# Performance work log

Hardware: AMD Instinct MI355X
Metric: run time of the kernel (lower is better)

Reference implementation:

```python
import jax, jax.numpy as jnp
import numpy as np


def setup_inputs() -> dict:
    key = jax.random.key(0)
    k1, k2 = jax.random.split(key)
    B, C, H, W = 8, 19, 512, 1024
    preds = jax.random.normal(k1, (B, C, H, W), dtype=jnp.float32)
    targets = jax.random.randint(k2, (B, H, W), 0, C, dtype=jnp.int32)
    return {"preds": preds, "targets": targets}


def reference(preds, targets):
    # preds: [B, C, H, W] logits; targets: [B, H, W] int class labels
    C = preds.shape[1]
    # softmax over class dim (does not change argmax but kept for faithfulness)
    probs = jax.nn.softmax(preds, axis=1)
    pred_lab = jnp.argmax(probs, axis=1)  # [B, H, W]

    p = pred_lab.ravel().astype(jnp.int32)
    t = targets.ravel().astype(jnp.int32)

    # single-pass histograms replacing the per-class Python loop
    pred_count = jnp.bincount(p, length=C)                      # |pred == c|
    true_count = jnp.bincount(t, length=C)                      # |true == c|
    # intersection: count matches routed to their class, mismatches to bin C
    inter = jnp.bincount(jnp.where(p == t, p, C), length=C + 1)[:C]

    union = pred_count + true_count - inter
    iou_all = jnp.where(
        true_count > 0,
        inter.astype(jnp.float32) / jnp.maximum(union, 1).astype(jnp.float32),
        jnp.float32(0.0),
    )
    # original loop iterates classes 1..C-1 (skips class 0 / background)
    iou = iou_all[1:]
    mean_iou = jnp.mean(iou)
    return iou, mean_iou
```

## Files before the change

### kernel.cpp

```cpp
#include <hip/hip_runtime.h>

#define NCLASS 19
#define NCNT   (3 * NCLASS)
#define HW (512 * 1024)
#define NB 8
#define NPIX (NB * HW)
#define NGROUP (NPIX / 4)
#define GROUPS_PER_BLOCK 512
#define GRID (NGROUP / GROUPS_PER_BLOCK)

typedef float v4f __attribute__((ext_vector_type(4)));
typedef int   v4i __attribute__((ext_vector_type(4)));
typedef unsigned int v4u __attribute__((ext_vector_type(4)));


__global__ __launch_bounds__(256) void iou_count_kernel(
    const float* __restrict__ preds,
    const int* __restrict__ targets,
    unsigned int* __restrict__ partials)
{
    __shared__ unsigned int s_cnt[NCNT];

    const int t = threadIdx.x;
    if (t < NCNT) s_cnt[t] = 0u;
    __syncthreads();

    const int gblk = blockIdx.x * GROUPS_PER_BLOCK;
    const int p0   = gblk << 2;
    const int b    = p0 >> 19;
    const int hw   = p0 & (HW - 1);

    const v4f* __restrict__ base =
        (const v4f*)(preds + (size_t)b * NCLASS * HW + hw) + t;
    const size_t plane4 = HW / 4;

    v4f m0 = __builtin_nontemporal_load(&base[0]);
    v4f m1 = __builtin_nontemporal_load(&base[256]);
    int i0x = 0, i0y = 0, i0z = 0, i0w = 0;
    int i1x = 0, i1y = 0, i1z = 0, i1w = 0;

    #pragma unroll
    for (int c = 1; c < NCLASS; ++c) {
        const v4f a = __builtin_nontemporal_load(&base[(size_t)c * plane4]);
        const v4f d = __builtin_nontemporal_load(&base[(size_t)c * plane4 + 256]);
        if (a.x > m0.x) { m0.x = a.x; i0x = c; }
        if (a.y > m0.y) { m0.y = a.y; i0y = c; }
        if (a.z > m0.z) { m0.z = a.z; i0z = c; }
        if (a.w > m0.w) { m0.w = a.w; i0w = c; }
        if (d.x > m1.x) { m1.x = d.x; i1x = c; }
        if (d.y > m1.y) { m1.y = d.y; i1y = c; }
        if (d.z > m1.z) { m1.z = d.z; i1z = c; }
        if (d.w > m1.w) { m1.w = d.w; i1w = c; }
    }

    const v4i* __restrict__ tgt4 = (const v4i*)targets + gblk + t;
    const v4i ta = __builtin_nontemporal_load(&tgt4[0]);
    const v4i tb = __builtin_nontemporal_load(&tgt4[256]);

    atomicAdd(&s_cnt[i0x], 1u);
    atomicAdd(&s_cnt[i0y], 1u);
    atomicAdd(&s_cnt[i0z], 1u);
    atomicAdd(&s_cnt[i0w], 1u);
    atomicAdd(&s_cnt[i1x], 1u);
    atomicAdd(&s_cnt[i1y], 1u);
    atomicAdd(&s_cnt[i1z], 1u);
    atomicAdd(&s_cnt[i1w], 1u);

    atomicAdd(&s_cnt[NCLASS + ta.x], 1u);
    atomicAdd(&s_cnt[NCLASS + ta.y], 1u);
    atomicAdd(&s_cnt[NCLASS + ta.z], 1u);
    atomicAdd(&s_cnt[NCLASS + ta.w], 1u);
    atomicAdd(&s_cnt[NCLASS + tb.x], 1u);
    atomicAdd(&s_cnt[NCLASS + tb.y], 1u);
    atomicAdd(&s_cnt[NCLASS + tb.z], 1u);
    atomicAdd(&s_cnt[NCLASS + tb.w], 1u);

    if (i0x == ta.x) atomicAdd(&s_cnt[2 * NCLASS + i0x], 1u);
    if (i0y == ta.y) atomicAdd(&s_cnt[2 * NCLASS + i0y], 1u);
    if (i0z == ta.z) atomicAdd(&s_cnt[2 * NCLASS + i0z], 1u);
    if (i0w == ta.w) atomicAdd(&s_cnt[2 * NCLASS + i0w], 1u);
    if (i1x == tb.x) atomicAdd(&s_cnt[2 * NCLASS + i1x], 1u);
    if (i1y == tb.y) atomicAdd(&s_cnt[2 * NCLASS + i1y], 1u);
    if (i1z == tb.z) atomicAdd(&s_cnt[2 * NCLASS + i1z], 1u);
    if (i1w == tb.w) atomicAdd(&s_cnt[2 * NCLASS + i1w], 1u);

    __syncthreads();
    if (t < NCNT) partials[t * GRID + blockIdx.x] = s_cnt[t];
}

__global__ __launch_bounds__(1024) void iou_finalize_kernel(
    const unsigned int* __restrict__ partials,
    float* __restrict__ out)
{
    __shared__ unsigned int s_red[NCNT][16];
    __shared__ unsigned int s_tot[NCNT];
    __shared__ float s_iou[NCLASS];

    const int t = threadIdx.x;
    const int j = t >> 4;
    const int k = t & 15;

    if (j < NCNT) {
        const v4u* __restrict__ p4 = (const v4u*)(partials + j * GRID);
        unsigned int s = 0;
        #pragma unroll
        for (int i = 0; i < 32; ++i) {
            const v4u v = p4[i * 16 + k];
            s += v.x + v.y + v.z + v.w;
        }
        s_red[j][k] = s;
    }
    __syncthreads();
    if (j < NCNT && k == 0) {
        unsigned int s = 0;
        #pragma unroll
        for (int i = 0; i < 16; ++i) s += s_red[j][i];
        s_tot[j] = s;
    }
    __syncthreads();

    if (t < NCLASS) {
        const unsigned int pc = s_tot[t];
        const unsigned int tc = s_tot[NCLASS + t];
        const unsigned int ic = s_tot[2 * NCLASS + t];
        const unsigned int un = pc + tc - ic;
        const unsigned int und = un > 1u ? un : 1u;
        const float iou = (tc > 0u) ? ((float)ic / (float)und) : 0.0f;
        s_iou[t] = iou;
        if (t >= 1) out[t - 1] = iou;
    }
    __syncthreads();
    if (t == 0) {
        float s = 0.0f;
        for (int c = 1; c < NCLASS; ++c) s += s_iou[c];
        out[NCLASS - 1] = s / (float)(NCLASS - 1);
    }
}

extern "C" void kernel_launch(void* const* d_in, const int* in_sizes, int n_in,
                              void* d_out, int out_size, void* d_ws, size_t ws_size,
                              hipStream_t stream) {
    const float* preds  = (const float*)d_in[0];
    const int* targets  = (const int*)d_in[1];
    float* out          = (float*)d_out;
    unsigned int* partials = (unsigned int*)d_ws;

    iou_count_kernel<<<GRID, 256, 0, stream>>>(preds, targets, partials);
    iou_finalize_kernel<<<1, 1024, 0, stream>>>(partials, out);
}
```

Before: 404.8 us.

## Issue all class loads up front and reduce counts via replicated global atomics

Each thread now handles one 4-pixel group and issues all 19 class-plane loads before the argmax, so more memory requests are in flight per thread. The grid doubles to 8192 blocks and an occupancy hint is added to launch bounds. The per-block partials array and the tree reduction are replaced by atomic adds into 16 replicated global counters, which a tiny zero kernel clears and a small finalize kernel sums. This costs one extra kernel launch, more global atomics and a finalize with divergent barriers and a stray dead load.

```diff
diff --git a/kernel.cpp b/kernel.cpp
--- a/kernel.cpp
+++ b/kernel.cpp
@@ -6,18 +6,24 @@
 #define NB 8
 #define NPIX (NB * HW)
 #define NGROUP (NPIX / 4)
-#define GROUPS_PER_BLOCK 512
-#define GRID (NGROUP / GROUPS_PER_BLOCK)
+#define GPB 256
+#define GRID (NGROUP / GPB)
+#define NREP 16
 
 typedef float v4f __attribute__((ext_vector_type(4)));
 typedef int   v4i __attribute__((ext_vector_type(4)));
-typedef unsigned int v4u __attribute__((ext_vector_type(4)));
 
 
-__global__ __launch_bounds__(256) void iou_count_kernel(
+__global__ __launch_bounds__(1024) void iou_zero_kernel(unsigned int* __restrict__ acc)
+{
+    const int t = threadIdx.x;
+    if (t < NREP * NCNT) acc[t] = 0u;
+}
+
+__global__ __launch_bounds__(256, 4) void iou_count_kernel(
     const float* __restrict__ preds,
     const int* __restrict__ targets,
-    unsigned int* __restrict__ partials)
+    unsigned int* __restrict__ acc)
 {
     __shared__ unsigned int s_cnt[NCNT];
 
@@ -25,109 +31,78 @@
     if (t < NCNT) s_cnt[t] = 0u;
     __syncthreads();
 
-    const int gblk = blockIdx.x * GROUPS_PER_BLOCK;
-    const int p0   = gblk << 2;
-    const int b    = p0 >> 19;
-    const int hw   = p0 & (HW - 1);
+    const int g  = blockIdx.x * GPB + t;
+    const int p0 = g << 2;
+    const int b  = p0 >> 19;
+    const int hw = p0 & (HW - 1);
+    const size_t plane4 = HW / 4;
 
     const v4f* __restrict__ base =
-        (const v4f*)(preds + (size_t)b * NCLASS * HW + hw) + t;
-    const size_t plane4 = HW / 4;
+        (const v4f*)(preds + (size_t)b * NCLASS * HW) + (hw >> 2);
 
-    v4f m0 = __builtin_nontemporal_load(&base[0]);
-    v4f m1 = __builtin_nontemporal_load(&base[256]);
-    int i0x = 0, i0y = 0, i0z = 0, i0w = 0;
-    int i1x = 0, i1y = 0, i1z = 0, i1w = 0;
+    v4f v[NCLASS];
+    #pragma unroll
+    for (int c = 0; c < NCLASS; ++c)
+        v[c] = __builtin_nontemporal_load(&base[(size_t)c * plane4]);
 
+    v4f m = v[0];
+    int ix = 0, iy = 0, iz = 0, iw = 0;
     #pragma unroll
     for (int c = 1; c < NCLASS; ++c) {
-        const v4f a = __builtin_nontemporal_load(&base[(size_t)c * plane4]);
-        const v4f d = __builtin_nontemporal_load(&base[(size_t)c * plane4 + 256]);
-        if (a.x > m0.x) { m0.x = a.x; i0x = c; }
-        if (a.y > m0.y) { m0.y = a.y; i0y = c; }
-        if (a.z > m0.z) { m0.z = a.z; i0z = c; }
-        if (a.w > m0.w) { m0.w = a.w; i0w = c; }
-        if (d.x > m1.x) { m1.x = d.x; i1x = c; }
-        if (d.y > m1.y) { m1.y = d.y; i1y = c; }
-        if (d.z > m1.z) { m1.z = d.z; i1z = c; }
-        if (d.w > m1.w) { m1.w = d.w; i1w = c; }
+        if (v[c].x > m.x) { m.x = v[c].x; ix = c; }
+        if (v[c].y > m.y) { m.y = v[c].y; iy = c; }
+        if (v[c].z > m.z) { m.z = v[c].z; iz = c; }
+        if (v[c].w > m.w) { m.w = v[c].w; iw = c; }
     }
 
-    const v4i* __restrict__ tgt4 = (const v4i*)targets + gblk + t;
-    const v4i ta = __builtin_nontemporal_load(&tgt4[0]);
-    const v4i tb = __builtin_nontemporal_load(&tgt4[256]);
+    const v4i ta = __builtin_nontemporal_load(&((const v4i*)targets)[g]);
 
-    atomicAdd(&s_cnt[i0x], 1u);
-    atomicAdd(&s_cnt[i0y], 1u);
-    atomicAdd(&s_cnt[i0z], 1u);
-    atomicAdd(&s_cnt[i0w], 1u);
-    atomicAdd(&s_cnt[i1x], 1u);
-    atomicAdd(&s_cnt[i1y], 1u);
-    atomicAdd(&s_cnt[i1z], 1u);
-    atomicAdd(&s_cnt[i1w], 1u);
+    atomicAdd(&s_cnt[ix], 1u);
+    atomicAdd(&s_cnt[iy], 1u);
+    atomicAdd(&s_cnt[iz], 1u);
+    atomicAdd(&s_cnt[iw], 1u);
 
     atomicAdd(&s_cnt[NCLASS + ta.x], 1u);
     atomicAdd(&s_cnt[NCLASS + ta.y], 1u);
     atomicAdd(&s_cnt[NCLASS + ta.z], 1u);
     atomicAdd(&s_cnt[NCLASS + ta.w], 1u);
-    atomicAdd(&s_cnt[NCLASS + tb.x], 1u);
-    atomicAdd(&s_cnt[NCLASS + tb.y], 1u);
-    atomicAdd(&s_cnt[NCLASS + tb.z], 1u);
-    atomicAdd(&s_cnt[NCLASS + tb.w], 1u);
 
-    if (i0x == ta.x) atomicAdd(&s_cnt[2 * NCLASS + i0x], 1u);
-    if (i0y == ta.y) atomicAdd(&s_cnt[2 * NCLASS + i0y], 1u);
-    if (i0z == ta.z) atomicAdd(&s_cnt[2 * NCLASS + i0z], 1u);
-    if (i0w == ta.w) atomicAdd(&s_cnt[2 * NCLASS + i0w], 1u);
-    if (i1x == tb.x) atomicAdd(&s_cnt[2 * NCLASS + i1x], 1u);
-    if (i1y == tb.y) atomicAdd(&s_cnt[2 * NCLASS + i1y], 1u);
-    if (i1z == tb.z) atomicAdd(&s_cnt[2 * NCLASS + i1z], 1u);
-    if (i1w == tb.w) atomicAdd(&s_cnt[2 * NCLASS + i1w], 1u);
+    if (ix == ta.x) atomicAdd(&s_cnt[2 * NCLASS + ix], 1u);
+    if (iy == ta.y) atomicAdd(&s_cnt[2 * NCLASS + iy], 1u);
+    if (iz == ta.z) atomicAdd(&s_cnt[2 * NCLASS + iz], 1u);
+    if (iw == ta.w) atomicAdd(&s_cnt[2 * NCLASS + iw], 1u);
 
     __syncthreads();
-    if (t < NCNT) partials[t * GRID + blockIdx.x] = s_cnt[t];
+    if (t < NCNT) atomicAdd(&acc[(blockIdx.x & (NREP - 1)) * NCNT + t], s_cnt[t]);
 }
 
-__global__ __launch_bounds__(1024) void iou_finalize_kernel(
-    const unsigned int* __restrict__ partials,
+__global__ __launch_bounds__(64) void iou_finalize_kernel(
+    const unsigned int* __restrict__ acc,
     float* __restrict__ out)
 {
-    __shared__ unsigned int s_red[NCNT][16];
-    __shared__ unsigned int s_tot[NCNT];
     __shared__ float s_iou[NCLASS];
+    const int t = threadIdx.x;
 
-    const int t = threadIdx.x;
-    const int j = t >> 4;
-    const int k = t & 15;
-
-    if (j < NCNT) {
-        const v4u* __restrict__ p4 = (const v4u*)(partials + j * GRID);
+    if (t < NCNT) {
         unsigned int s = 0;
         #pragma unroll
-        for (int i = 0; i < 32; ++i) {
-            const v4u v = p4[i * 16 + k];
-            s += v.x + v.y + v.z + v.w;
+        for (int r = 0; r < NREP; ++r) s += acc[r * NCNT + t];
+        ((unsigned int*)s_iou)[0];
+        __shared__ unsigned int s_tot[NCNT];
+        s_tot[t] = s;
+        __syncthreads();
+        if (t < NCLASS) {
+            const unsigned int pc = s_tot[t];
+            const unsigned int tc = s_tot[NCLASS + t];
+            const unsigned int ic = s_tot[2 * NCLASS + t];
+            unsigned int un = pc + tc - ic;
+            un = un > 1u ? un : 1u;
+            const float iou = (tc > 0u) ? ((float)ic / (float)un) : 0.0f;
+            s_iou[t] = iou;
+            if (t >= 1) out[t - 1] = iou;
         }
-        s_red[j][k] = s;
-    }
-    __syncthreads();
-    if (j < NCNT && k == 0) {
-        unsigned int s = 0;
-        #pragma unroll
-        for (int i = 0; i < 16; ++i) s += s_red[j][i];
-        s_tot[j] = s;
-    }
-    __syncthreads();
-
-    if (t < NCLASS) {
-        const unsigned int pc = s_tot[t];
-        const unsigned int tc = s_tot[NCLASS + t];
-        const unsigned int ic = s_tot[2 * NCLASS + t];
-        const unsigned int un = pc + tc - ic;
-        const unsigned int und = un > 1u ? un : 1u;
-        const float iou = (tc > 0u) ? ((float)ic / (float)und) : 0.0f;
-        s_iou[t] = iou;
-        if (t >= 1) out[t - 1] = iou;
+    } else {
+        __syncthreads();
     }
     __syncthreads();
     if (t == 0) {
@@ -143,8 +118,9 @@
     const float* preds  = (const float*)d_in[0];
     const int* targets  = (const int*)d_in[1];
     float* out          = (float*)d_out;
-    unsigned int* partials = (unsigned int*)d_ws;
+    unsigned int* acc   = (unsigned int*)d_ws;
 
-    iou_count_kernel<<<GRID, 256, 0, stream>>>(preds, targets, partials);
-    iou_finalize_kernel<<<1, 1024, 0, stream>>>(partials, out);
+    iou_zero_kernel<<<1, 1024, 0, stream>>>(acc);
+    iou_count_kernel<<<GRID, 256, 0, stream>>>(preds, targets, acc);
+    iou_finalize_kernel<<<1, 64, 0, stream>>>(acc, out);
 }
```

Measured after the change: 403.3 us. No clear change (-0.4%).
